# Kernel optimization log

Measured on AMD Instinct MI355X. Metric: run time of the kernel, lower is better.

Reference implementation:

```python
import jax, jax.numpy as jnp
import numpy as np

WS = (7, 7)   # window size
SS = (3, 3)   # shift size
NH = 3        # num heads
EPS = 1e-5


def _rel_index():
    # relative position index [N, N], computed exactly as in WindowAttention.__init__
    coords = np.stack(np.meshgrid(np.arange(WS[0]), np.arange(WS[1]), indexing='ij'))  # [2,7,7]
    cf = coords.reshape(2, -1)                     # [2, N]
    rel = (cf[:, :, None] - cf[:, None, :]).transpose(1, 2, 0)  # [N, N, 2]
    rel[..., 0] += WS[0] - 1
    rel[..., 1] += WS[1] - 1
    idx = rel[..., 0] * (2 * WS[1] - 1) + rel[..., 1]
    return jnp.asarray(idx)


def _attn_mask(H, W):
    # standard Swin shifted-window mask: [nW, N, N] of {0, -100}
    img = np.zeros((H, W), dtype=np.float32)
    cnt = 0
    for hs in (slice(0, -WS[0]), slice(-WS[0], -SS[0]), slice(-SS[0], None)):
        for ws_ in (slice(0, -WS[1]), slice(-WS[1], -SS[1]), slice(-SS[1], None)):
            img[hs, ws_] = cnt
            cnt += 1
    mw = img.reshape(H // WS[0], WS[0], W // WS[1], WS[1]).transpose(0, 2, 1, 3)
    mw = mw.reshape(-1, WS[0] * WS[1])            # [nW, N]
    am = mw[:, None, :] - mw[:, :, None]
    am = np.where(am != 0, np.float32(-100.0), np.float32(0.0))
    return jnp.asarray(am)


def _ln(x, g, b):
    m = x.mean(-1, keepdims=True)
    v = ((x - m) ** 2).mean(-1, keepdims=True)
    return (x - m) * jax.lax.rsqrt(v + EPS) * g + b


def _forward(x, norm1_g, norm1_b, qkv_w, qkv_b, rel_table, proj_w, proj_b,
             norm2_g, norm2_b, mlp_w1, mlp_b1, mlp_w2, mlp_b2):
    B, C, H, W = x.shape
    N = WS[0] * WS[1]
    hd = C // NH
    scale = hd ** -0.5

    # norm1 over channels (token layout [B, HW, C])
    xt = x.reshape(B, C, H * W).transpose(0, 2, 1)
    xn = _ln(xt, norm1_g, norm1_b).transpose(0, 2, 1).reshape(B, C, H, W)

    # cyclic shift + window partition -> [B*nW, N, C]
    shifted = jnp.roll(xn, (-SS[0], -SS[1]), axis=(2, 3))
    nWh, nWw = H // WS[0], W // WS[1]
    xw = shifted.transpose(0, 2, 3, 1)  # [B, H, W, C]
    xwin = xw.reshape(B, nWh, WS[0], nWw, WS[1], C).transpose(0, 1, 3, 2, 4, 5)
    xwin = xwin.reshape(-1, N, C)

    # windowed attention with relative position bias + shift mask
    qkv = (xwin @ qkv_w.T + qkv_b).reshape(-1, N, 3, NH, hd).transpose(2, 0, 3, 1, 4)
    q, k, v = qkv[0] * scale, qkv[1], qkv[2]            # [B_, h, N, hd]
    attn = jnp.einsum('bhnd,bhmd->bhnm', q, k)          # [B_, h, N, N]
    bias = rel_table[_rel_index()]                       # [N, N, h]
    attn = attn + bias.transpose(2, 0, 1)[None]
    mask = _attn_mask(H, W)                              # [nW, N, N]
    nW = mask.shape[0]
    attn = attn.reshape(-1, nW, NH, N, N) + mask[None, :, None]
    attn = jax.nn.softmax(attn.reshape(-1, NH, N, N), axis=-1)
    out = jnp.einsum('bhnm,bhmd->bhnd', attn, v).transpose(0, 2, 1, 3).reshape(-1, N, C)
    out = out @ proj_w.T + proj_b

    # window reverse + reverse shift -> [B, C, H, W]
    xr = out.reshape(B, nWh, nWw, WS[0], WS[1], C).transpose(0, 1, 3, 2, 4, 5)
    xr = xr.reshape(B, H, W, C).transpose(0, 3, 1, 2)
    xr = jnp.roll(xr, (SS[0], SS[1]), axis=(2, 3))

    x = x + xr  # residual (drop_path = Identity)

    # MLP branch with pre-norm over channels
    xt = x.reshape(B, C, H * W).transpose(0, 2, 1)
    h = _ln(xt, norm2_g, norm2_b)
    h = jax.nn.gelu(h @ mlp_w1.T + mlp_b1, approximate=False)
    h = h @ mlp_w2.T + mlp_b2
    return x + h.transpose(0, 2, 1).reshape(B, C, H, W)


def setup_inputs() -> dict:
    key = jax.random.key(0)
    ks = jax.random.split(key, 8)
    B, C, H, W = 8, 96, 224, 224
    hid = 384
    s = 0.02
    return {
        'x': jax.random.normal(ks[0], (B, C, H, W), jnp.float32),
        'norm1_g': jnp.ones((C,), jnp.float32),
        'norm1_b': jnp.zeros((C,), jnp.float32),
        'qkv_w': jax.random.normal(ks[1], (3 * C, C), jnp.float32) * s,
        'qkv_b': jnp.zeros((3 * C,), jnp.float32),
        'rel_table': jax.random.normal(ks[2], (169, NH), jnp.float32) * s,
        'proj_w': jax.random.normal(ks[3], (C, C), jnp.float32) * s,
        'proj_b': jnp.zeros((C,), jnp.float32),
        'norm2_g': jnp.ones((C,), jnp.float32),
        'norm2_b': jnp.zeros((C,), jnp.float32),
        'mlp_w1': jax.random.normal(ks[4], (hid, C), jnp.float32) * s,
        'mlp_b1': jnp.zeros((hid,), jnp.float32),
        'mlp_w2': jax.random.normal(ks[5], (C, hid), jnp.float32) * s,
        'mlp_b2': jnp.zeros((C,), jnp.float32),
    }


def reference(x, norm1_g, norm1_b, qkv_w, qkv_b, rel_table, proj_w, proj_b,
              norm2_g, norm2_b, mlp_w1, mlp_b1, mlp_w2, mlp_b2):
    return _forward(x, norm1_g, norm1_b, qkv_w, qkv_b, rel_table, proj_w, proj_b,
                    norm2_g, norm2_b, mlp_w1, mlp_b1, mlp_w2, mlp_b2)
```

## Files before the change

### kernel.cpp

```cpp
#include <hip/hip_runtime.h>
#include <hip/hip_bf16.h>

typedef __attribute__((ext_vector_type(8))) short short8;
typedef __attribute__((ext_vector_type(4))) short s16x4;
typedef __attribute__((ext_vector_type(4))) float f32x4;

#define D_H   224
#define D_W   224
#define D_HW  50176
#define SCALE 0.17677669529663687f

#define WO_QKVW  0
#define WO_PROJW 27648
#define WO_W1    36864
#define WO_W2    73728
#define WO_TOT   110592

#define XT_SH 0
#define YT_SH 38535168
#define W_SH  77070336
#define WS_NEED ((size_t)(77070336 + 110592) * 2)

static __device__ __forceinline__ short f2s(float v) {
    union { __hip_bfloat16 b; short s; } u; u.b = __float2bfloat16(v); return u.s;
}
static __device__ __forceinline__ float s2f(short s) {
    union { short s; __hip_bfloat16 b; } u; u.s = s; return __bfloat162float(u.b);
}

#define MFMA(a, b, c) __builtin_amdgcn_mfma_f32_16x16x32_bf16((a), (b), (c), 0, 0, 0)

static __device__ __forceinline__ short8 normfrag(const short* p, const float* g,
                                                  const float* b, int c0, float m, float rs) {
    short8 r = *(const short8*)p;
    short8 o;
#pragma unroll
    for (int j = 0; j < 8; j++) o[j] = f2s((s2f(r[j]) - m) * rs * g[c0 + j] + b[c0 + j]);
    return o;
}

__global__ __launch_bounds__(256) void k_prep(
    const float* __restrict__ qkvw, const float* __restrict__ projw,
    const float* __restrict__ w1, const float* __restrict__ w2, short* __restrict__ ws)
{
    int i4 = blockIdx.x * 256 + threadIdx.x;
    const float* src; int off;
    if (i4 < 6912)        { src = qkvw;  off = 0; }
    else if (i4 < 9216)   { src = projw; off = 6912; }
    else if (i4 < 18432)  { src = w1;    off = 9216; }
    else                  { src = w2;    off = 18432; }
    f32x4 v = *(const f32x4*)&src[(i4 - off) * 4];
    s16x4 s;
#pragma unroll
    for (int j = 0; j < 4; j++) s[j] = f2s(v[j]);
    *(s16x4*)&ws[i4 * 4] = s;
}

__global__ __launch_bounds__(256) void k_t(const float* __restrict__ x, short* __restrict__ xt)
{
    __shared__ short tile[224][96];
    const int tid = threadIdx.x;
    const int bh = blockIdx.x;
    const int b = bh / 224, h = bh - b * 224;
    const int pbase = (b * 96) * D_HW + h * 224;

#pragma unroll
    for (int k = 0; k < 21; k++) {
        int idx = tid + k * 256;
        int w = idx % 224, u = idx / 224;
        int c0 = u * 4;
        s16x4 v;
        v[0] = f2s(x[pbase + (c0 + 0) * D_HW + w]);
        v[1] = f2s(x[pbase + (c0 + 1) * D_HW + w]);
        v[2] = f2s(x[pbase + (c0 + 2) * D_HW + w]);
        v[3] = f2s(x[pbase + (c0 + 3) * D_HW + w]);
        int slot = (u + w) % 24;
        *(s16x4*)&tile[w][slot * 4] = v;
    }
    __syncthreads();
    const int obase = ((b * 224 + h) * 224) * 96;
#pragma unroll
    for (int k = 0; k < 11; k++) {
        int idx = tid + k * 256;
        if (idx < 2688) {
            int w = idx / 12, s = idx - w * 12;
            int sl0 = (s * 2 + w) % 24, sl1 = (s * 2 + 1 + w) % 24;
            s16x4 a = *(const s16x4*)&tile[w][sl0 * 4];
            s16x4 c = *(const s16x4*)&tile[w][sl1 * 4];
            short8 o;
            o[0] = a[0]; o[1] = a[1]; o[2] = a[2]; o[3] = a[3];
            o[4] = c[0]; o[5] = c[1]; o[6] = c[2]; o[7] = c[3];
            *(short8*)&xt[obase + w * 96 + s * 8] = o;
        }
    }
}

__global__ __launch_bounds__(256, 3) void k_attn_t(
    const short* __restrict__ xt, const float* __restrict__ n1g, const float* __restrict__ n1b,
    const float* __restrict__ qkvb, const float* __restrict__ relt,
    const float* __restrict__ projb, const short* __restrict__ wsw, short* __restrict__ yt)
{
    __shared__ short qk[64][200];
    __shared__ short vt[96][72];
    __shared__ __align__(16) short xs[64][104];
    short (*ps)[72] = (short(*)[72])xs;
    __shared__ int   cnt_s[64];
    __shared__ float mean_s[64], rstd_s[64];

    const int tid  = threadIdx.x;
    const int wave = tid >> 6, lane = tid & 63;
    const int l16  = lane & 15, q8 = (lane >> 4) * 8, q4 = (lane >> 4) * 4;
    const int t0   = wave * 16;

    const short* qkvw_bf  = wsw + WO_QKVW;
    const short* projw_bf = wsw + WO_PROJW;

    const int wi = blockIdx.x;
    const int b  = wi >> 10, nw = wi & 1023;
    const int wh = nw >> 5, ww = nw & 31;
    const bool edge = (wh == 31) || (ww == 31);

    if (tid < 64) {
        int t = (tid < 49) ? tid : 48;
        int r = t / 7, c = t - r * 7;
        int sh = wh * 7 + r, sw = ww * 7 + c;
        int rh = (sh < 217) ? 0 : ((sh < 221) ? 1 : 2);
        int rw = (sw < 217) ? 0 : ((sw < 221) ? 1 : 2);
        cnt_s[tid] = rh * 3 + rw;
    }
#pragma unroll
    for (int k = 0; k < 3; k++) {
        int idx = tid + k * 256;
        int t = idx / 12, s = idx - t * 12;
        short8 v = {0, 0, 0, 0, 0, 0, 0, 0};
        if (t < 49) {
            int r = t / 7, cc = t - r * 7;
            int hh = wh * 7 + r + 3;  if (hh >= D_H) hh -= D_H;
            int w2 = ww * 7 + cc + 3; if (w2 >= D_W) w2 -= D_W;
            v = *(const short8*)&xt[((b * 224 + hh) * 224 + w2) * 96 + s * 8];
        }
        *(short8*)&xs[t][s * 8] = v;
    }
    __syncthreads();

    {
        int t = tid >> 2, p = tid & 3;
        float s = 0.f, s2 = 0.f;
#pragma unroll
        for (int i = 0; i < 6; i++) {
            s16x4 v4 = *(const s16x4*)&xs[t][p * 24 + i * 4];
#pragma unroll
            for (int j = 0; j < 4; j++) { float v = s2f(v4[j]); s += v; s2 += v * v; }
        }
        s += __shfl_xor(s, 1); s2 += __shfl_xor(s2, 1);
        s += __shfl_xor(s, 2); s2 += __shfl_xor(s2, 2);
        if (p == 0) {
            float m = s * (1.f / 96.f);
            float var = s2 * (1.f / 96.f) - m * m;
            mean_s[t] = m; rstd_s[t] = rsqrtf(var + 1e-5f);
        }
    }
    __syncthreads();

    const float m0 = mean_s[t0 + l16], rs0 = rstd_s[t0 + l16];
    short8 a0 = normfrag(&xs[t0 + l16][q8],      n1g, n1b, q8,      m0, rs0);
    short8 a1 = normfrag(&xs[t0 + l16][32 + q8], n1g, n1b, 32 + q8, m0, rs0);
    short8 a2 = normfrag(&xs[t0 + l16][64 + q8], n1g, n1b, 64 + q8, m0, rs0);

#pragma unroll
    for (int jc = 0; jc < 3; jc++) {
#pragma unroll
        for (int nt = 0; nt < 6; nt++) {
            int jj = nt * 16 + l16;
            const short* wr = qkvw_bf + (jc * 96 + jj) * 96;
            f32x4 acc = {0.f, 0.f, 0.f, 0.f};
            acc = MFMA(a0, *(const short8*)&wr[q8],      acc);
            acc = MFMA(a1, *(const short8*)&wr[32 + q8], acc);
            acc = MFMA(a2, *(const short8*)&wr[64 + q8], acc);
            float bias = qkvb[jc * 96 + jj];
            if (jc == 0) {
#pragma unroll
                for (int r = 0; r < 4; r++) qk[t0 + q4 + r][jj] = f2s((acc[r] + bias) * SCALE);
            } else if (jc == 1) {
#pragma unroll
                for (int r = 0; r < 4; r++) qk[t0 + q4 + r][96 + jj] = f2s(acc[r] + bias);
            } else {
                s16x4 v4;
#pragma unroll
                for (int r = 0; r < 4; r++) v4[r] = f2s(acc[r] + bias);
                *(s16x4*)&vt[jj][t0 + q4] = v4;
            }
        }
    }

    float biasv[4][4][3];
#pragma unroll
    for (int nt = 0; nt < 4; nt++) {
        int m  = nt * 16 + l16;
        int mm = (m < 49) ? m : 48;
        int r2 = mm / 7, c2 = mm - r2 * 7;
        int cm = cnt_s[m];
#pragma unroll
        for (int r = 0; r < 4; r++) {
            int n  = t0 + q4 + r;
            int nn = (n < 49) ? n : 48;
            int r1 = nn / 7, c1 = nn - r1 * 7;
            int ri = ((r1 - r2 + 6) * 13 + (c1 - c2 + 6)) * 3;
            float mk = (edge && (cnt_s[n] != cm)) ? -100.f : 0.f;
            biasv[nt][r][0] = relt[ri + 0] + mk;
            biasv[nt][r][1] = relt[ri + 1] + mk;
            biasv[nt][r][2] = relt[ri + 2] + mk;
        }
    }
    const bool inval3 = (l16 != 0);

#pragma unroll
    for (int h = 0; h < 3; h++) {
        __syncthreads();
        short8 aq = *(const short8*)&qk[t0 + l16][h * 32 + q8];
        f32x4 sv[4];
#pragma unroll
        for (int nt = 0; nt < 4; nt++) {
            f32x4 z = {0.f, 0.f, 0.f, 0.f};
            sv[nt] = MFMA(aq, *(const short8*)&qk[nt * 16 + l16][96 + h * 32 + q8], z);
        }
        float mx[4] = {-1e30f, -1e30f, -1e30f, -1e30f};
#pragma unroll
        for (int nt = 0; nt < 4; nt++) {
#pragma unroll
            for (int r = 0; r < 4; r++) {
                float v = sv[nt][r] + biasv[nt][r][h];
                if (nt == 3 && inval3) v = -1e30f;
                sv[nt][r] = v;
                mx[r] = fmaxf(mx[r], v);
            }
        }
#pragma unroll
        for (int d = 1; d < 16; d <<= 1) {
#pragma unroll
            for (int r = 0; r < 4; r++) mx[r] = fmaxf(mx[r], __shfl_xor(mx[r], d));
        }
        float sm[4] = {0.f, 0.f, 0.f, 0.f};
#pragma unroll
        for (int nt = 0; nt < 4; nt++) {
#pragma unroll
            for (int r = 0; r < 4; r++) {
                float e = (nt == 3 && inval3) ? 0.f : __expf(sv[nt][r] - mx[r]);
                sv[nt][r] = e;
                sm[r] += e;
            }
        }
#pragma unroll
        for (int d = 1; d < 16; d <<= 1) {
#pragma unroll
            for (int r = 0; r < 4; r++) sm[r] += __shfl_xor(sm[r], d);
        }
        float inv[4];
#pragma unroll
        for (int r = 0; r < 4; r++) inv[r] = 1.f / sm[r];
#pragma unroll
        for (int nt = 0; nt < 4; nt++) {
#pragma unroll
            for (int r = 0; r < 4; r++)
                ps[t0 + q4 + r][nt * 16 + l16] = f2s(sv[nt][r] * inv[r]);
        }
        __syncthreads();
        short8 p0 = *(const short8*)&ps[t0 + l16][q8];
        short8 p1 = *(const short8*)&ps[t0 + l16][32 + q8];
#pragma unroll
        for (int nt = 0; nt < 2; nt++) {
            f32x4 acc = {0.f, 0.f, 0.f, 0.f};
            acc = MFMA(p0, *(const short8*)&vt[h * 32 + nt * 16 + l16][q8],      acc);
            acc = MFMA(p1, *(const short8*)&vt[h * 32 + nt * 16 + l16][32 + q8], acc);
            int d = nt * 16 + l16;
#pragma unroll
            for (int r = 0; r < 4; r++) {
                int t = t0 + q4 + r;
                if (t < 49) qk[t][h * 32 + d] = f2s(acc[r]);
            }
        }
    }

    __syncthreads();
    short8 o0 = *(const short8*)&qk[t0 + l16][q8];
    short8 o1 = *(const short8*)&qk[t0 + l16][32 + q8];
    short8 o2 = *(const short8*)&qk[t0 + l16][64 + q8];
    __syncthreads();
#pragma unroll
    for (int nt = 0; nt < 6; nt++) {
        int i = nt * 16 + l16;
        const short* wr = projw_bf + i * 96;
        f32x4 acc = {0.f, 0.f, 0.f, 0.f};
        acc = MFMA(o0, *(const short8*)&wr[q8],      acc);
        acc = MFMA(o1, *(const short8*)&wr[32 + q8], acc);
        acc = MFMA(o2, *(const short8*)&wr[64 + q8], acc);
        float pb = projb[i];
#pragma unroll
        for (int r = 0; r < 4; r++) {
            int t = t0 + q4 + r;
            if (t < 49) qk[t][i] = f2s(acc[r] + pb);
        }
    }
    __syncthreads();
#pragma unroll
    for (int k = 0; k < 3; k++) {
        int idx = tid + k * 256;
        if (idx < 588) {
            int t = idx / 12, s = idx - t * 12;
            int r = t / 7, cc = t - r * 7;
            int hh = wh * 7 + r + 3;  if (hh >= D_H) hh -= D_H;
            int w2 = ww * 7 + cc + 3; if (w2 >= D_W) w2 -= D_W;
            *(short8*)&yt[((b * 224 + hh) * 224 + w2) * 96 + s * 8] =
                *(const short8*)&qk[t][s * 8];
        }
    }
}

#define XCOL(row, c) ((((((c) >> 3) ^ (((row) >> 2) & 7)) << 3)) | ((c) & 7))

__global__ __launch_bounds__(256, 3) void k_mlp_t(
    const float* __restrict__ x, const short* __restrict__ ytk, float* __restrict__ y,
    const float* __restrict__ n2g, const float* __restrict__ n2b,
    const float* __restrict__ b1, const float* __restrict__ b2, const short* __restrict__ wsw)
{
    __shared__ __align__(16) short xs[64][128];
    __shared__ __align__(16) short wb[96][104];
    __shared__ __align__(16) short hb[64][104];
    __shared__ float mean_s[64], rstd_s[64];

    const int tid  = threadIdx.x;
    const int wave = tid >> 6, lane = tid & 63;
    const int l16  = lane & 15, q8 = (lane >> 4) * 8, q4 = (lane >> 4) * 4;
    const int t0   = wave * 16;

    const short* w1_bf = wsw + WO_W1;
    const short* w2_bf = wsw + WO_W2;

    const int T0 = blockIdx.x * 64;
    const int b  = T0 / D_HW;
    const int p0 = T0 - b * D_HW;
    const int base = (b * 96) * D_HW + p0;

#pragma unroll
    for (int k = 0; k < 3; k++) {
        int idx = tid + k * 256;
        int t = idx / 12, s = idx - t * 12;
        *(short8*)&xs[t][(s ^ ((t >> 2) & 7)) << 3] =
            *(const short8*)&ytk[(T0 + t) * 96 + s * 8];
    }
    __syncthreads();

    float yv[6][4];
#pragma unroll
    for (int k = 0; k < 6; k++) {
        int idx = tid + k * 256;
        int c = idx >> 4, q = idx & 15;
        f32x4 xv = *(const f32x4*)&x[base + c * D_HW + q * 4];
        int ch = ((c >> 3) ^ (q & 7)) * 8 + (c & 7);
#pragma unroll
        for (int j = 0; j < 4; j++) {
            float v = xv[j] + s2f(xs[q * 4 + j][ch]);
            yv[k][j] = v;
            xs[q * 4 + j][ch] = f2s(v);
        }
    }
    __syncthreads();

    {
        int t = tid >> 2, p = tid & 3;
        float s = 0.f, s2 = 0.f;
#pragma unroll
        for (int i = 0; i < 6; i++) {
            int c = p * 24 + i * 4;
            s16x4 v4 = *(const s16x4*)&xs[t][XCOL(t, c)];
#pragma unroll
            for (int j = 0; j < 4; j++) { float v = s2f(v4[j]); s += v; s2 += v * v; }
        }
        s += __shfl_xor(s, 1); s2 += __shfl_xor(s2, 1);
        s += __shfl_xor(s, 2); s2 += __shfl_xor(s2, 2);
        if (p == 0) {
            float m = s * (1.f / 96.f);
            float var = s2 * (1.f / 96.f) - m * m;
            mean_s[t] = m; rstd_s[t] = rsqrtf(var + 1e-5f);
        }
    }
    __syncthreads();

    short8 xa[3];
    {
        int t = t0 + l16;
        float m = mean_s[t], rs = rstd_s[t];
        int key = (t >> 2) & 7;
#pragma unroll
        for (int kk = 0; kk < 3; kk++) {
            int ch = kk * 4 + (lane >> 4);
            xa[kk] = normfrag(&xs[t][(ch ^ key) << 3], n2g, n2b, ch * 8, m, rs);
        }
    }

    f32x4 c2[6];
#pragma unroll
    for (int nt = 0; nt < 6; nt++) c2[nt] = (f32x4){0.f, 0.f, 0.f, 0.f};

    for (int jc = 0; jc < 4; jc++) {
        __syncthreads();
#pragma unroll
        for (int k = 0; k < 5; k++) {
            int idx = tid + k * 256;
            if (idx < 1152) {
                int j2 = idx / 12, s = idx - j2 * 12;
                *(short8*)&wb[j2][s * 8] = *(const short8*)&w1_bf[(jc * 96 + j2) * 96 + s * 8];
            }
        }
        __syncthreads();
#pragma unroll
        for (int nt = 0; nt < 6; nt++) {
            int jj = nt * 16 + l16;
            f32x4 acc = {0.f, 0.f, 0.f, 0.f};
            acc = MFMA(xa[0], *(const short8*)&wb[jj][q8],      acc);
            acc = MFMA(xa[1], *(const short8*)&wb[jj][32 + q8], acc);
            acc = MFMA(xa[2], *(const short8*)&wb[jj][64 + q8], acc);
            float bb = b1[jc * 96 + jj];
#pragma unroll
            for (int r = 0; r < 4; r++) {
                float v = acc[r] + bb;
                float g = 0.5f * v * (1.f + erff(v * 0.7071067811865475f));
                hb[t0 + q4 + r][jj] = f2s(g);
            }
        }
        __syncthreads();
#pragma unroll
        for (int k = 0; k < 5; k++) {
            int idx = tid + k * 256;
            if (idx < 1152) {
                int o = idx / 12, s = idx - o * 12;
                *(short8*)&wb[o][s * 8] = *(const short8*)&w2_bf[o * 384 + jc * 96 + s * 8];
            }
        }
        __syncthreads();
        {
            short8 h0 = *(const short8*)&hb[t0 + l16][q8];
            short8 h1 = *(const short8*)&hb[t0 + l16][32 + q8];
            short8 h2 = *(const short8*)&hb[t0 + l16][64 + q8];
#pragma unroll
            for (int nt = 0; nt < 6; nt++) {
                int jj = nt * 16 + l16;
                c2[nt] = MFMA(h0, *(const short8*)&wb[jj][q8],      c2[nt]);
                c2[nt] = MFMA(h1, *(const short8*)&wb[jj][32 + q8], c2[nt]);
                c2[nt] = MFMA(h2, *(const short8*)&wb[jj][64 + q8], c2[nt]);
            }
        }
    }
    __syncthreads();

#pragma unroll
    for (int nt = 0; nt < 6; nt++) {
        int i = nt * 16 + l16;
        float bo = b2[i];
#pragma unroll
        for (int r = 0; r < 4; r++) {
            int t = t0 + q4 + r;
            xs[t][XCOL(t, i)] = f2s(bo + c2[nt][r]);
        }
    }
    __syncthreads();
#pragma unroll
    for (int k = 0; k < 6; k++) {
        int idx = tid + k * 256;
        int c = idx >> 4, q = idx & 15;
        int ch = ((c >> 3) ^ (q & 7)) * 8 + (c & 7);
        f32x4 o;
#pragma unroll
        for (int j = 0; j < 4; j++) o[j] = yv[k][j] + s2f(xs[q * 4 + j][ch]);
        *(f32x4*)&y[base + c * D_HW + q * 4] = o;
    }
}

__global__ __launch_bounds__(256, 3) void k_attn_f(
    const float* __restrict__ x, const float* __restrict__ n1g, const float* __restrict__ n1b,
    const float* __restrict__ qkvb, const float* __restrict__ relt,
    const float* __restrict__ projb, const short* __restrict__ wsw, float* __restrict__ y)
{
    __shared__ short qk[64][200];
    __shared__ short vt[96][72];
    __shared__ __align__(16) short xs[64][104];
    short (*ps)[72] = (short(*)[72])xs;
    __shared__ int   cnt_s[64];
    __shared__ float mean_s[64], rstd_s[64];

    const int tid  = threadIdx.x;
    const int wave = tid >> 6, lane = tid & 63;
    const int l16  = lane & 15, q8 = (lane >> 4) * 8, q4 = (lane >> 4) * 4;
    const int t0   = wave * 16;

    const short* qkvw_bf  = wsw + WO_QKVW;
    const short* projw_bf = wsw + WO_PROJW;

    const int wi = blockIdx.x;
    const int b  = wi >> 10, nw = wi & 1023;
    const int wh = nw >> 5, ww = nw & 31;
    const bool edge = (wh == 31) || (ww == 31);

    if (tid < 64) {
        int t = (tid < 49) ? tid : 48;
        int r = t / 7, c = t - r * 7;
        int sh = wh * 7 + r, sw = ww * 7 + c;
        int rh = (sh < 217) ? 0 : ((sh < 221) ? 1 : 2);
        int rw = (sw < 217) ? 0 : ((sw < 221) ? 1 : 2);
        cnt_s[tid] = rh * 3 + rw;
    }
    {
        int t = lane;
        int r = t / 7, cc = t - r * 7;
        int hh = wh * 7 + r + 3;  if (hh >= D_H) hh -= D_H;
        int w2 = ww * 7 + cc + 3; if (w2 >= D_W) w2 -= D_W;
        int off0 = (b * 96) * D_HW + hh * D_W + w2;
#pragma unroll
        for (int n = 0; n < 6; n++) {
            int c0 = wave * 24 + n * 4;
            s16x4 v4 = {0, 0, 0, 0};
            if (t < 49) {
                v4[0] = f2s(x[off0 + (c0 + 0) * D_HW]);
                v4[1] = f2s(x[off0 + (c0 + 1) * D_HW]);
                v4[2] = f2s(x[off0 + (c0 + 2) * D_HW]);
                v4[3] = f2s(x[off0 + (c0 + 3) * D_HW]);
            }
            *(s16x4*)&xs[t][c0] = v4;
        }
    }
    __syncthreads();
    {
        int t = tid >> 2, p = tid & 3;
        float s = 0.f, s2 = 0.f;
#pragma unroll
        for (int i = 0; i < 6; i++) {
            s16x4 v4 = *(const s16x4*)&xs[t][p * 24 + i * 4];
#pragma unroll
            for (int j = 0; j < 4; j++) { float v = s2f(v4[j]); s += v; s2 += v * v; }
        }
        s += __shfl_xor(s, 1); s2 += __shfl_xor(s2, 1);
        s += __shfl_xor(s, 2); s2 += __shfl_xor(s2, 2);
        if (p == 0) {
            float m = s * (1.f / 96.f);
            float var = s2 * (1.f / 96.f) - m * m;
            mean_s[t] = m; rstd_s[t] = rsqrtf(var + 1e-5f);
        }
    }
    __syncthreads();

    const float m0 = mean_s[t0 + l16], rs0 = rstd_s[t0 + l16];
    short8 a0 = normfrag(&xs[t0 + l16][q8],      n1g, n1b, q8,      m0, rs0);
    short8 a1 = normfrag(&xs[t0 + l16][32 + q8], n1g, n1b, 32 + q8, m0, rs0);
    short8 a2 = normfrag(&xs[t0 + l16][64 + q8], n1g, n1b, 64 + q8, m0, rs0);

#pragma unroll
    for (int jc = 0; jc < 3; jc++) {
#pragma unroll
        for (int nt = 0; nt < 6; nt++) {
            int jj = nt * 16 + l16;
            const short* wr = qkvw_bf + (jc * 96 + jj) * 96;
            f32x4 acc = {0.f, 0.f, 0.f, 0.f};
            acc = MFMA(a0, *(const short8*)&wr[q8],      acc);
            acc = MFMA(a1, *(const short8*)&wr[32 + q8], acc);
            acc = MFMA(a2, *(const short8*)&wr[64 + q8], acc);
            float bias = qkvb[jc * 96 + jj];
            if (jc == 0) {
#pragma unroll
                for (int r = 0; r < 4; r++) qk[t0 + q4 + r][jj] = f2s((acc[r] + bias) * SCALE);
            } else if (jc == 1) {
#pragma unroll
                for (int r = 0; r < 4; r++) qk[t0 + q4 + r][96 + jj] = f2s(acc[r] + bias);
            } else {
                s16x4 v4;
#pragma unroll
                for (int r = 0; r < 4; r++) v4[r] = f2s(acc[r] + bias);
                *(s16x4*)&vt[jj][t0 + q4] = v4;
            }
        }
    }

    float biasv[4][4][3];
#pragma unroll
    for (int nt = 0; nt < 4; nt++) {
        int m  = nt * 16 + l16;
        int mm = (m < 49) ? m : 48;
        int r2 = mm / 7, c2 = mm - r2 * 7;
        int cm = cnt_s[m];
#pragma unroll
        for (int r = 0; r < 4; r++) {
            int n  = t0 + q4 + r;
            int nn = (n < 49) ? n : 48;
            int r1 = nn / 7, c1 = nn - r1 * 7;
            int ri = ((r1 - r2 + 6) * 13 + (c1 - c2 + 6)) * 3;
            float mk = (edge && (cnt_s[n] != cm)) ? -100.f : 0.f;
            biasv[nt][r][0] = relt[ri + 0] + mk;
            biasv[nt][r][1] = relt[ri + 1] + mk;
            biasv[nt][r][2] = relt[ri + 2] + mk;
        }
    }
    const bool inval3 = (l16 != 0);

#pragma unroll
    for (int h = 0; h < 3; h++) {
        __syncthreads();
        short8 aq = *(const short8*)&qk[t0 + l16][h * 32 + q8];
        f32x4 sv[4];
#pragma unroll
        for (int nt = 0; nt < 4; nt++) {
            f32x4 z = {0.f, 0.f, 0.f, 0.f};
            sv[nt] = MFMA(aq, *(const short8*)&qk[nt * 16 + l16][96 + h * 32 + q8], z);
        }
        float mx[4] = {-1e30f, -1e30f, -1e30f, -1e30f};
#pragma unroll
        for (int nt = 0; nt < 4; nt++) {
#pragma unroll
            for (int r = 0; r < 4; r++) {
                float v = sv[nt][r] + biasv[nt][r][h];
                if (nt == 3 && inval3) v = -1e30f;
                sv[nt][r] = v;
                mx[r] = fmaxf(mx[r], v);
            }
        }
#pragma unroll
        for (int d = 1; d < 16; d <<= 1) {
#pragma unroll
            for (int r = 0; r < 4; r++) mx[r] = fmaxf(mx[r], __shfl_xor(mx[r], d));
        }
        float sm[4] = {0.f, 0.f, 0.f, 0.f};
#pragma unroll
        for (int nt = 0; nt < 4; nt++) {
#pragma unroll
            for (int r = 0; r < 4; r++) {
                float e = (nt == 3 && inval3) ? 0.f : __expf(sv[nt][r] - mx[r]);
                sv[nt][r] = e;
                sm[r] += e;
            }
        }
#pragma unroll
        for (int d = 1; d < 16; d <<= 1) {
#pragma unroll
            for (int r = 0; r < 4; r++) sm[r] += __shfl_xor(sm[r], d);
        }
        float inv[4];
#pragma unroll
        for (int r = 0; r < 4; r++) inv[r] = 1.f / sm[r];
#pragma unroll
        for (int nt = 0; nt < 4; nt++) {
#pragma unroll
            for (int r = 0; r < 4; r++)
                ps[t0 + q4 + r][nt * 16 + l16] = f2s(sv[nt][r] * inv[r]);
        }
        __syncthreads();
        short8 p0 = *(const short8*)&ps[t0 + l16][q8];
        short8 p1 = *(const short8*)&ps[t0 + l16][32 + q8];
#pragma unroll
        for (int nt = 0; nt < 2; nt++) {
            f32x4 acc = {0.f, 0.f, 0.f, 0.f};
            acc = MFMA(p0, *(const short8*)&vt[h * 32 + nt * 16 + l16][q8],      acc);
            acc = MFMA(p1, *(const short8*)&vt[h * 32 + nt * 16 + l16][32 + q8], acc);
            int d = nt * 16 + l16;
#pragma unroll
            for (int r = 0; r < 4; r++) {
                int t = t0 + q4 + r;
                if (t < 49) qk[t][h * 32 + d] = f2s(acc[r]);
            }
        }
    }

    __syncthreads();
    short8 o0 = *(const short8*)&qk[t0 + l16][q8];
    short8 o1 = *(const short8*)&qk[t0 + l16][32 + q8];
    short8 o2 = *(const short8*)&qk[t0 + l16][64 + q8];
    int  po[4];
    bool tv[4];
#pragma unroll
    for (int r = 0; r < 4; r++) {
        int t = t0 + q4 + r;
        tv[r] = (t < 49);
        int tt = tv[r] ? t : 0;
        int rr = tt / 7, cc = tt - rr * 7;
        int hh = wh * 7 + rr + 3;  if (hh >= D_H) hh -= D_H;
        int w2 = ww * 7 + cc + 3;  if (w2 >= D_W) w2 -= D_W;
        po[r] = (b * 96) * D_HW + hh * D_W + w2;
    }
#pragma unroll
    for (int nt = 0; nt < 6; nt++) {
        int i = nt * 16 + l16;
        const short* wr = projw_bf + i * 96;
        f32x4 acc = {0.f, 0.f, 0.f, 0.f};
        acc = MFMA(o0, *(const short8*)&wr[q8],      acc);
        acc = MFMA(o1, *(const short8*)&wr[32 + q8], acc);
        acc = MFMA(o2, *(const short8*)&wr[64 + q8], acc);
        float pb = projb[i];
#pragma unroll
        for (int r = 0; r < 4; r++) {
            if (tv[r]) {
                int off = po[r] + i * D_HW;
                y[off] = x[off] + acc[r] + pb;
            }
        }
    }
}

__global__ __launch_bounds__(256, 3) void k_mlp_f(
    float* __restrict__ y, const float* __restrict__ n2g, const float* __restrict__ n2b,
    const float* __restrict__ b1, const float* __restrict__ b2, const short* __restrict__ wsw)
{
    __shared__ short xs[128][104];
    __shared__ short hb[128][104];
    __shared__ float mean_s[128], rstd_s[128];

    const int tid  = threadIdx.x;
    const int wave = tid >> 6, lane = tid & 63;
    const int l16  = lane & 15, q8 = (lane >> 4) * 8, q4 = (lane >> 4) * 4;
    const int t0   = wave * 32;

    const short* w1_bf = wsw + WO_W1;
    const short* w2_bf = wsw + WO_W2;

    const int T0 = blockIdx.x * 128;
    const int b  = T0 / D_HW;
    const int p0 = T0 - b * D_HW;
    const int base = (b * 96) * D_HW + p0;

    for (int idx = tid; idx < 96 * 32; idx += 256) {
        int c = idx >> 5, q = idx & 31;
        f32x4 v4 = *(const f32x4*)&y[base + c * D_HW + q * 4];
        xs[q * 4 + 0][c] = f2s(v4[0]);
        xs[q * 4 + 1][c] = f2s(v4[1]);
        xs[q * 4 + 2][c] = f2s(v4[2]);
        xs[q * 4 + 3][c] = f2s(v4[3]);
    }
    __syncthreads();
    {
        int t = tid >> 1, p = tid & 1;
        float s = 0.f, s2 = 0.f;
#pragma unroll
        for (int i = 0; i < 12; i++) {
            s16x4 v4 = *(const s16x4*)&xs[t][p * 48 + i * 4];
#pragma unroll
            for (int j = 0; j < 4; j++) { float v = s2f(v4[j]); s += v; s2 += v * v; }
        }
        s += __shfl_xor(s, 1); s2 += __shfl_xor(s2, 1);
        float m = s * (1.f / 96.f);
        float var = s2 * (1.f / 96.f) - m * m;
        mean_s[t] = m; rstd_s[t] = rsqrtf(var + 1e-5f);
    }
    __syncthreads();

    short8 xa[2][3];
#pragma unroll
    for (int s = 0; s < 2; s++) {
        float m = mean_s[t0 + s * 16 + l16], rs = rstd_s[t0 + s * 16 + l16];
#pragma unroll
        for (int kk = 0; kk < 3; kk++)
            xa[s][kk] = normfrag(&xs[t0 + s * 16 + l16][kk * 32 + q8], n2g, n2b,
                                 kk * 32 + q8, m, rs);
    }

    f32x4 c2[2][6];
#pragma unroll
    for (int s = 0; s < 2; s++)
#pragma unroll
        for (int nt = 0; nt < 6; nt++) c2[s][nt] = (f32x4){0.f, 0.f, 0.f, 0.f};

    for (int jc = 0; jc < 4; jc++) {
#pragma unroll
        for (int s = 0; s < 2; s++) {
#pragma unroll
            for (int nt = 0; nt < 6; nt++) {
                int jj = nt * 16 + l16;
                const short* wr = w1_bf + (jc * 96 + jj) * 96;
                f32x4 acc = {0.f, 0.f, 0.f, 0.f};
                acc = MFMA(xa[s][0], *(const short8*)&wr[q8],      acc);
                acc = MFMA(xa[s][1], *(const short8*)&wr[32 + q8], acc);
                acc = MFMA(xa[s][2], *(const short8*)&wr[64 + q8], acc);
                float bb = b1[jc * 96 + jj];
#pragma unroll
                for (int r = 0; r < 4; r++) {
                    float v = acc[r] + bb;
                    float g = 0.5f * v * (1.f + erff(v * 0.7071067811865475f));
                    hb[t0 + s * 16 + q4 + r][jj] = f2s(g);
                }
            }
        }
        __syncthreads();
#pragma unroll
        for (int s = 0; s < 2; s++) {
            short8 h0 = *(const short8*)&hb[t0 + s * 16 + l16][q8];
            short8 h1 = *(const short8*)&hb[t0 + s * 16 + l16][32 + q8];
            short8 h2 = *(const short8*)&hb[t0 + s * 16 + l16][64 + q8];
#pragma unroll
            for (int nt = 0; nt < 6; nt++) {
                const short* wr = w2_bf + (nt * 16 + l16) * 384 + jc * 96;
                c2[s][nt] = MFMA(h0, *(const short8*)&wr[q8],      c2[s][nt]);
                c2[s][nt] = MFMA(h1, *(const short8*)&wr[32 + q8], c2[s][nt]);
                c2[s][nt] = MFMA(h2, *(const short8*)&wr[64 + q8], c2[s][nt]);
            }
        }
        __syncthreads();
    }

#pragma unroll
    for (int s = 0; s < 2; s++)
#pragma unroll
        for (int nt = 0; nt < 6; nt++) {
            int i = nt * 16 + l16;
            float bo = b2[i];
#pragma unroll
            for (int r = 0; r < 4; r++)
                xs[t0 + s * 16 + q4 + r][i] = f2s(bo + c2[s][nt][r]);
        }
    __syncthreads();
    for (int idx = tid; idx < 96 * 32; idx += 256) {
        int c = idx >> 5, q = idx & 31;
        int off = base + c * D_HW + q * 4;
        f32x4 v4 = *(const f32x4*)&y[off];
        v4[0] += s2f(xs[q * 4 + 0][c]);
        v4[1] += s2f(xs[q * 4 + 1][c]);
        v4[2] += s2f(xs[q * 4 + 2][c]);
        v4[3] += s2f(xs[q * 4 + 3][c]);
        *(f32x4*)&y[off] = v4;
    }
}

extern "C" void kernel_launch(void* const* d_in, const int* in_sizes, int n_in,
                              void* d_out, int out_size, void* d_ws, size_t ws_size,
                              hipStream_t stream) {
    const float* x    = (const float*)d_in[0];
    const float* n1g  = (const float*)d_in[1];
    const float* n1b  = (const float*)d_in[2];
    const float* qkvw = (const float*)d_in[3];
    const float* qkvb = (const float*)d_in[4];
    const float* relt = (const float*)d_in[5];
    const float* projw= (const float*)d_in[6];
    const float* projb= (const float*)d_in[7];
    const float* n2g  = (const float*)d_in[8];
    const float* n2b  = (const float*)d_in[9];
    const float* w1   = (const float*)d_in[10];
    const float* b1   = (const float*)d_in[11];
    const float* w2   = (const float*)d_in[12];
    const float* b2   = (const float*)d_in[13];
    float* y  = (float*)d_out;
    short* ws = (short*)d_ws;

    if (ws_size >= WS_NEED) {
        short* xt  = ws + XT_SH;
        short* ytk = ws + YT_SH;
        short* wbf = ws + W_SH;
        k_prep<<<108, 256, 0, stream>>>(qkvw, projw, w1, w2, wbf);
        k_t<<<1792, 256, 0, stream>>>(x, xt);
        k_attn_t<<<8192, 256, 0, stream>>>(xt, n1g, n1b, qkvb, relt, projb, wbf, ytk);
        k_mlp_t<<<6272, 256, 0, stream>>>(x, ytk, y, n2g, n2b, b1, b2, wbf);
    } else {
        k_prep<<<108, 256, 0, stream>>>(qkvw, projw, w1, w2, ws);
        k_attn_f<<<8192, 256, 0, stream>>>(x, n1g, n1b, qkvb, relt, projb, ws, y);
        k_mlp_f<<<3136, 256, 0, stream>>>(y, n2g, n2b, b1, b2, ws);
    }
}
```

Before: 751.4 us.

## Drop block barriers, read MLP weights from global, use fast erf and rcp

The MLP kernel no longer stages W1/W2 tiles in shared memory. Each wave reads weight fragments straight from global or cache, which removes four barriers per chunk and the wb buffer, and launch bounds are raised to 4 blocks per SM. In the attention kernel, barriers around wave-private rows are removed, and the x and vt shared buffers are aliased into one region to cut LDS use. erff is replaced with an Abramowitz-Stegun polynomial approximation and 1/x with the hardware rcp. The risks are more global/L2 traffic for weights and small precision differences.

```diff
diff --git a/kernel.cpp b/kernel.cpp
--- a/kernel.cpp
+++ b/kernel.cpp
@@ -37,6 +37,15 @@
 #pragma unroll
     for (int j = 0; j < 8; j++) o[j] = f2s((s2f(r[j]) - m) * rs * g[c0 + j] + b[c0 + j]);
     return o;
+}
+
+static __device__ __forceinline__ float erf_fast(float x) {
+    float a = fabsf(x);
+    float t = __builtin_amdgcn_rcpf(1.f + 0.3275911f * a);
+    float p = t * (0.254829592f + t * (-0.284496736f + t * (1.421413741f +
+              t * (-1.453152027f + t * 1.061405429f))));
+    float y = 1.f - p * __expf(-a * a);
+    return copysignf(y, x);
 }
 
 __global__ __launch_bounds__(256) void k_prep(
@@ -101,9 +110,10 @@
     const float* __restrict__ projb, const short* __restrict__ wsw, short* __restrict__ yt)
 {
     __shared__ short qk[64][200];
-    __shared__ short vt[96][72];
-    __shared__ __align__(16) short xs[64][104];
-    short (*ps)[72] = (short(*)[72])xs;
+    __shared__ __align__(16) short region[11520];
+    short (*xs)[104] = (short(*)[104])region;
+    short (*ps)[72]  = (short(*)[72])region;
+    short (*vt)[72]  = (short(*)[72])(region + 4608);
     __shared__ int   cnt_s[64];
     __shared__ float mean_s[64], rstd_s[64];
 
@@ -160,12 +170,12 @@
             mean_s[t] = m; rstd_s[t] = rsqrtf(var + 1e-5f);
         }
     }
-    __syncthreads();
 
     const float m0 = mean_s[t0 + l16], rs0 = rstd_s[t0 + l16];
     short8 a0 = normfrag(&xs[t0 + l16][q8],      n1g, n1b, q8,      m0, rs0);
     short8 a1 = normfrag(&xs[t0 + l16][32 + q8], n1g, n1b, 32 + q8, m0, rs0);
     short8 a2 = normfrag(&xs[t0 + l16][64 + q8], n1g, n1b, 64 + q8, m0, rs0);
+    __syncthreads();
 
 #pragma unroll
     for (int jc = 0; jc < 3; jc++) {
@@ -214,9 +224,10 @@
     }
     const bool inval3 = (l16 != 0);
 
+    __syncthreads();
+
 #pragma unroll
     for (int h = 0; h < 3; h++) {
-        __syncthreads();
         short8 aq = *(const short8*)&qk[t0 + l16][h * 32 + q8];
         f32x4 sv[4];
 #pragma unroll
@@ -257,14 +268,13 @@
         }
         float inv[4];
 #pragma unroll
-        for (int r = 0; r < 4; r++) inv[r] = 1.f / sm[r];
+        for (int r = 0; r < 4; r++) inv[r] = __builtin_amdgcn_rcpf(sm[r]);
 #pragma unroll
         for (int nt = 0; nt < 4; nt++) {
 #pragma unroll
             for (int r = 0; r < 4; r++)
                 ps[t0 + q4 + r][nt * 16 + l16] = f2s(sv[nt][r] * inv[r]);
         }
-        __syncthreads();
         short8 p0 = *(const short8*)&ps[t0 + l16][q8];
         short8 p1 = *(const short8*)&ps[t0 + l16][32 + q8];
 #pragma unroll
@@ -281,11 +291,9 @@
         }
     }
 
-    __syncthreads();
     short8 o0 = *(const short8*)&qk[t0 + l16][q8];
     short8 o1 = *(const short8*)&qk[t0 + l16][32 + q8];
     short8 o2 = *(const short8*)&qk[t0 + l16][64 + q8];
-    __syncthreads();
 #pragma unroll
     for (int nt = 0; nt < 6; nt++) {
         int i = nt * 16 + l16;
@@ -318,13 +326,12 @@
 
 #define XCOL(row, c) ((((((c) >> 3) ^ (((row) >> 2) & 7)) << 3)) | ((c) & 7))
 
-__global__ __launch_bounds__(256, 3) void k_mlp_t(
+__global__ __launch_bounds__(256, 4) void k_mlp_t(
     const float* __restrict__ x, const short* __restrict__ ytk, float* __restrict__ y,
     const float* __restrict__ n2g, const float* __restrict__ n2b,
     const float* __restrict__ b1, const float* __restrict__ b2, const short* __restrict__ wsw)
 {
     __shared__ __align__(16) short xs[64][128];
-    __shared__ __align__(16) short wb[96][104];
     __shared__ __align__(16) short hb[64][104];
     __shared__ float mean_s[64], rstd_s[64];
 
@@ -384,7 +391,6 @@
             mean_s[t] = m; rstd_s[t] = rsqrtf(var + 1e-5f);
         }
     }
-    __syncthreads();
 
     short8 xa[3];
     {
@@ -402,56 +408,37 @@
 #pragma unroll
     for (int nt = 0; nt < 6; nt++) c2[nt] = (f32x4){0.f, 0.f, 0.f, 0.f};
 
+#pragma unroll
     for (int jc = 0; jc < 4; jc++) {
-        __syncthreads();
-#pragma unroll
-        for (int k = 0; k < 5; k++) {
-            int idx = tid + k * 256;
-            if (idx < 1152) {
-                int j2 = idx / 12, s = idx - j2 * 12;
-                *(short8*)&wb[j2][s * 8] = *(const short8*)&w1_bf[(jc * 96 + j2) * 96 + s * 8];
-            }
-        }
-        __syncthreads();
 #pragma unroll
         for (int nt = 0; nt < 6; nt++) {
             int jj = nt * 16 + l16;
+            const short* wr = w1_bf + (jc * 96 + jj) * 96;
             f32x4 acc = {0.f, 0.f, 0.f, 0.f};
-            acc = MFMA(xa[0], *(const short8*)&wb[jj][q8],      acc);
-            acc = MFMA(xa[1], *(const short8*)&wb[jj][32 + q8], acc);
-            acc = MFMA(xa[2], *(const short8*)&wb[jj][64 + q8], acc);
+            acc = MFMA(xa[0], *(const short8*)&wr[q8],      acc);
+            acc = MFMA(xa[1], *(const short8*)&wr[32 + q8], acc);
+            acc = MFMA(xa[2], *(const short8*)&wr[64 + q8], acc);
             float bb = b1[jc * 96 + jj];
 #pragma unroll
             for (int r = 0; r < 4; r++) {
                 float v = acc[r] + bb;
-                float g = 0.5f * v * (1.f + erff(v * 0.7071067811865475f));
+                float g = 0.5f * v * (1.f + erf_fast(v * 0.7071067811865475f));
                 hb[t0 + q4 + r][jj] = f2s(g);
             }
         }
-        __syncthreads();
-#pragma unroll
-        for (int k = 0; k < 5; k++) {
-            int idx = tid + k * 256;
-            if (idx < 1152) {
-                int o = idx / 12, s = idx - o * 12;
-                *(short8*)&wb[o][s * 8] = *(const short8*)&w2_bf[o * 384 + jc * 96 + s * 8];
-            }
-        }
-        __syncthreads();
         {
             short8 h0 = *(const short8*)&hb[t0 + l16][q8];
             short8 h1 = *(const short8*)&hb[t0 + l16][32 + q8];
             short8 h2 = *(const short8*)&hb[t0 + l16][64 + q8];
 #pragma unroll
             for (int nt = 0; nt < 6; nt++) {
-                int jj = nt * 16 + l16;
-                c2[nt] = MFMA(h0, *(const short8*)&wb[jj][q8],      c2[nt]);
-                c2[nt] = MFMA(h1, *(const short8*)&wb[jj][32 + q8], c2[nt]);
-                c2[nt] = MFMA(h2, *(const short8*)&wb[jj][64 + q8], c2[nt]);
-            }
-        }
-    }
-    __syncthreads();
+                const short* wr = w2_bf + (nt * 16 + l16) * 384 + jc * 96;
+                c2[nt] = MFMA(h0, *(const short8*)&wr[q8],      c2[nt]);
+                c2[nt] = MFMA(h1, *(const short8*)&wr[32 + q8], c2[nt]);
+                c2[nt] = MFMA(h2, *(const short8*)&wr[64 + q8], c2[nt]);
+            }
+        }
+    }
 
 #pragma unroll
     for (int nt = 0; nt < 6; nt++) {
```

New measurement: 838.4 us. +11.6%, slower.
